# Kernel optimization log

Hardware: AMD Instinct MI355X
Metric: run time of the kernel (lower is better)

## Reference

```python
import jax, jax.numpy as jnp
import numpy as np
import math

MODEL_DIM = 1024
BATCH = 4
SEQ = 2048


def setup_inputs() -> dict:
    key = jax.random.key(0)
    kx, kq, kk, kv = jax.random.split(key, 4)
    x = jax.random.normal(kx, (BATCH, SEQ, MODEL_DIM), dtype=jnp.float32)
    # kaiming_uniform_(W.T, a=sqrt(5)) on a square matrix -> U(-b, b) with
    # b = sqrt(6 / ((1 + 5) * fan_in)) = 1/sqrt(model_dim)
    bound = 1.0 / math.sqrt(MODEL_DIM)
    Q = jax.random.uniform(kq, (MODEL_DIM, MODEL_DIM), jnp.float32, -bound, bound)
    K = jax.random.uniform(kk, (MODEL_DIM, MODEL_DIM), jnp.float32, -bound, bound)
    V = jax.random.uniform(kv, (MODEL_DIM, MODEL_DIM), jnp.float32, -bound, bound)
    # attention_input='both' => a = model_dim => F is the full identity mask
    F = jnp.eye(MODEL_DIM, dtype=jnp.float32)
    return {"x": x, "F": F, "Q": Q, "K": K, "V": V}


def reference(x, F, Q, K, V):
    # Qx = x @ F @ Q ; Kx = x @ F @ K ; Vx = x @ V
    xF = x @ F                      # [b, s, d]
    Qx = xF @ Q                     # [b, s, d]
    Kx = xF @ K                     # [b, s, d]
    Vx = x @ V                      # [b, s, d]
    scale = 1.0 / math.sqrt(MODEL_DIM)
    attn_scores = jnp.einsum('bsd,btd->bst', Qx, Kx) * scale  # [b, s, s]
    attn_probs = jax.nn.softmax(attn_scores, axis=-1)
    out = jnp.einsum('bst,btd->bsd', attn_probs, Vx)          # [b, s, d]
    return out
```

## Files before the change

### kernel.cpp

```cpp
#include <hip/hip_runtime.h>
#include <hip/hip_bf16.h>

using bf16 = __hip_bfloat16;
typedef __bf16 bf16x8 __attribute__((ext_vector_type(8)));
typedef float f32x4 __attribute__((ext_vector_type(4)));

#define AS3(p) ((__attribute__((address_space(3))) void*)(p))
#define AS1(p) ((const __attribute__((address_space(1))) void*)(p))

template <int W> __device__ __forceinline__ void waitv() {
  asm volatile("s_waitcnt vmcnt(%0)" ::"n"(W) : "memory");
}
#define BARR __builtin_amdgcn_s_barrier()
#define SCHEDB __builtin_amdgcn_sched_barrier(0)

__global__ void cast_f32_bf16_kernel(const float* __restrict__ in,
                                     bf16* __restrict__ out, int n4) {
  int i = blockIdx.x * blockDim.x + threadIdx.x;
  if (i >= n4) return;
  float4 v = reinterpret_cast<const float4*>(in)[i];
  union { ushort4 u; bf16 h[4]; } o;
  o.h[0] = __float2bfloat16(v.x);
  o.h[1] = __float2bfloat16(v.y);
  o.h[2] = __float2bfloat16(v.z);
  o.h[3] = __float2bfloat16(v.w);
  reinterpret_cast<ushort4*>(out)[i] = o.u;
}

__global__ void transpose3_kernel(const float* __restrict__ W0,
                                  const float* __restrict__ W1,
                                  const float* __restrict__ W2,
                                  bf16* __restrict__ out) {
  __shared__ bf16 tile[32][33];
  const float* in = (blockIdx.z == 0) ? W0 : (blockIdx.z == 1) ? W1 : W2;
  out += (long)blockIdx.z * 1024 * 1024;
  int c0 = blockIdx.x * 32, r0 = blockIdx.y * 32;
  for (int i = threadIdx.y; i < 32; i += 8)
    tile[i][threadIdx.x] = (bf16)in[(long)(r0 + i) * 1024 + c0 + threadIdx.x];
  __syncthreads();
  for (int i = threadIdx.y; i < 32; i += 8)
    out[(long)(c0 + i) * 1024 + r0 + threadIdx.x] = tile[threadIdx.x][i];
}

__device__ inline void store_c(float* p, float v) { *p = v; }
__device__ inline void store_c(bf16* p, float v) { *p = __float2bfloat16(v); }

template <int BN, int MODE, typename OutT>
__global__ __launch_bounds__(512, 1) void gemm2p_kernel(
    const bf16* __restrict__ A, const bf16* __restrict__ Bt, OutT* __restrict__ C,
    int K, int lda, int ldb, int ldc, long sAb, long sBb, long sCb,
    float* __restrict__ aux, int auxStride) {
  constexpr int BM = 256, BK = 64;
  constexpr int WN = (BN == 256) ? 4 : 2;
  constexpr int MF = (BN == 256) ? 8 : 4;
  constexpr int MCH = MF / 2;
  constexpr int NLA = 4;
  constexpr int NLB = BN / 64;
  constexpr int NL = NLA + NLB;
  constexpr int BUFELEM = (BM + BN) * BK;

  __shared__ alignas(16) bf16 lds[2 * BUFELEM];

  A += (long)blockIdx.z * sAb;
  Bt += (long)blockIdx.z * sBb;
  C += (long)blockIdx.z * sCb;
  if (MODE != 0) aux += (long)blockIdx.z * auxStride;
  const int tm = blockIdx.y * BM, tn = blockIdx.x * BN;
  const int tid = threadIdx.x, wv = tid >> 6, lane = tid & 63;
  const int wm = wv / WN, wn = wv % WN;
  const int r0 = wm * (MF * 16), c0 = wn * 64;
  const int lrow = lane & 15, lkc = lane >> 4;

  f32x4 acc[MF][4] = {};

  auto stage = [&](int buf, int kt) {
    bf16* base = lds + buf * BUFELEM;
#pragma unroll
    for (int i = 0; i < NLA; ++i) {
      int slot = i * 512 + tid;
      int row = slot >> 3;
      int cg = (slot & 7) ^ (row & 7);
      const bf16* src = A + (long)(tm + row) * lda + kt + cg * 8;
      __builtin_amdgcn_global_load_lds(AS1(src), AS3(base + slot * 8), 16, 0, 0);
    }
#pragma unroll
    for (int i = 0; i < NLB; ++i) {
      int slot = i * 512 + tid;
      int row = slot >> 3;
      int cg = (slot & 7) ^ (row & 7);
      const bf16* src = Bt + (long)(tn + row) * ldb + kt + cg * 8;
      __builtin_amdgcn_global_load_lds(AS1(src), AS3(base + BM * BK + slot * 8), 16, 0, 0);
    }
  };

  stage(0, 0);
  const int NT = K / BK;
  for (int t = 0; t < NT; ++t) {
    const int cur = t & 1;
    if (t + 1 < NT) {
      stage(cur ^ 1, (t + 1) * BK);
      waitv<NL>();
    } else {
      waitv<0>();
    }
    BARR;
    SCHEDB;

    const bf16* bA = lds + cur * BUFELEM;
    const bf16* bB = bA + BM * BK;

    bf16x8 bfr[4][2];
#pragma unroll
    for (int nj = 0; nj < 4; ++nj)
#pragma unroll
      for (int k = 0; k < 2; ++k) {
        int row = c0 + nj * 16 + lrow;
        int cx = (k * 4 + lkc) ^ (row & 7);
        bfr[nj][k] = *reinterpret_cast<const bf16x8*>(bB + row * 64 + cx * 8);
      }
#pragma unroll
    for (int ph = 0; ph < 2; ++ph) {
      bf16x8 afr[MCH][2];
#pragma unroll
      for (int mi = 0; mi < MCH; ++mi)
#pragma unroll
        for (int k = 0; k < 2; ++k) {
          int row = r0 + (ph * MCH + mi) * 16 + lrow;
          int cx = (k * 4 + lkc) ^ (row & 7);
          afr[mi][k] = *reinterpret_cast<const bf16x8*>(bA + row * 64 + cx * 8);
        }
      __builtin_amdgcn_s_setprio(1);
#pragma unroll
      for (int k = 0; k < 2; ++k)
#pragma unroll
        for (int mi = 0; mi < MCH; ++mi)
#pragma unroll
          for (int nj = 0; nj < 4; ++nj)
            acc[ph * MCH + mi][nj] = __builtin_amdgcn_mfma_f32_16x16x32_bf16(
                afr[mi][k], bfr[nj][k], acc[ph * MCH + mi][nj], 0, 0, 0);
      __builtin_amdgcn_s_setprio(0);
      SCHEDB;
      BARR;
      SCHEDB;
    }
  }

  const int crow = lkc * 4;
#pragma unroll
  for (int mi = 0; mi < MF; ++mi) {
#pragma unroll
    for (int r = 0; r < 4; ++r) {
      const int rowm = tm + r0 + mi * 16 + crow + r;
      OutT* cp = C + (long)rowm * ldc + tn + c0 + lrow;
      if (MODE == 0) {
#pragma unroll
        for (int nj = 0; nj < 4; ++nj) store_c(cp + nj * 16, acc[mi][nj][r]);
      } else if (MODE == 1) {
        float rs = 0.f;
#pragma unroll
        for (int nj = 0; nj < 4; ++nj) {
          float e = __expf(acc[mi][nj][r] * 0.03125f);
          rs += e;
          store_c(cp + nj * 16, e);
        }
        rs += __shfl_xor(rs, 1);
        rs += __shfl_xor(rs, 2);
        rs += __shfl_xor(rs, 4);
        rs += __shfl_xor(rs, 8);
        if ((lane & 15) == 0) atomicAdd(aux + rowm, rs);
      } else {
        float inv = 1.0f / aux[rowm];
#pragma unroll
        for (int nj = 0; nj < 4; ++nj) store_c(cp + nj * 16, acc[mi][nj][r] * inv);
      }
    }
  }
}

extern "C" void kernel_launch(void* const* d_in, const int* in_sizes, int n_in,
                              void* d_out, int out_size, void* d_ws, size_t ws_size,
                              hipStream_t stream) {
  const float* x = (const float*)d_in[0];
  const float* Wq = (const float*)d_in[2];
  const float* Wk = (const float*)d_in[3];
  const float* Wv = (const float*)d_in[4];
  float* out = (float*)d_out;

  const long D = 1024, S = 2048, B = 4, MS = B * S;

  bf16* xb  = (bf16*)d_ws;
  bf16* Wtc = xb + MS * D;
  bf16* QKx = Wtc + 3 * D * D;
  bf16* Vxt = QKx + MS * 2 * D;
  bf16* Sc  = Vxt + MS * D;
  float* rowsum = (float*)(Sc + B * S * S);

  dim3 blk(256);
  dim3 tblk(32, 8);

  cast_f32_bf16_kernel<<<(int)(MS * D / 4 / 256), blk, 0, stream>>>(x, xb, (int)(MS * D / 4));
  transpose3_kernel<<<dim3(32, 32, 3), tblk, 0, stream>>>(Wq, Wk, Wv, Wtc);
  gemm2p_kernel<128, 0, bf16><<<dim3(16, 32, 1), 512, 0, stream>>>(
      xb, Wtc, QKx, 1024, 1024, 1024, 2048, 0, 0, 0, nullptr, 0);
  gemm2p_kernel<128, 0, bf16><<<dim3(16, 4, 4), 512, 0, stream>>>(
      Wtc + 2 * D * D, xb, Vxt, 1024, 1024, 1024, 2048, 0, S * D, D * S, nullptr, 0);
  hipMemsetAsync(rowsum, 0, B * S * sizeof(float), stream);
  gemm2p_kernel<256, 1, bf16><<<dim3(8, 8, 4), 512, 0, stream>>>(
      QKx, QKx + D, Sc, 1024, 2048, 2048, 2048, S * 2 * D, S * 2 * D, S * S,
      rowsum, (int)S);
  gemm2p_kernel<128, 2, float><<<dim3(8, 8, 4), 512, 0, stream>>>(
      Sc, Vxt, out, 2048, 2048, 2048, 1024, S * S, D * S, S * D,
      rowsum, (int)S);
}
```

Before: 174.7 us.

## Add 256x256 GEMM kernel with 8-phase half-tile staging pipeline

Introduces a new GEMM kernel that splits each 256x256 tile's A and B k-slices into halves. Each half is staged separately, interleaving global-to-LDS loads with four MFMA phases and prefetching up to two k-steps ahead. It replaces the older kernel for the QK projection GEMM (now a 256-wide N tile) and for the score/exp GEMM. The aim is to hide load latency better and to increase reuse with larger tiles. The cost is more barriers per iteration and fewer blocks for the projection GEMM.

```diff
diff --git a/kernel.cpp b/kernel.cpp
--- a/kernel.cpp
+++ b/kernel.cpp
@@ -12,6 +12,7 @@
   asm volatile("s_waitcnt vmcnt(%0)" ::"n"(W) : "memory");
 }
 #define BARR __builtin_amdgcn_s_barrier()
+#define LGKM0 asm volatile("s_waitcnt lgkmcnt(0)" ::: "memory")
 #define SCHEDB __builtin_amdgcn_sched_barrier(0)
 
 __global__ void cast_f32_bf16_kernel(const float* __restrict__ in,
@@ -45,6 +46,160 @@
 __device__ inline void store_c(float* p, float v) { *p = v; }
 __device__ inline void store_c(bf16* p, float v) { *p = __float2bfloat16(v); }
 
+template <int MODE, typename OutT>
+__global__ __launch_bounds__(512, 1) void gemm8p_kernel(
+    const bf16* __restrict__ A, const bf16* __restrict__ Bt, OutT* __restrict__ C,
+    int K, int lda, int ldb, int ldc, long sAb, long sBb, long sCb,
+    float* __restrict__ aux, int auxStride) {
+  constexpr int HALF = 128 * 64;
+  constexpr int BB = 4 * HALF;
+  __shared__ alignas(16) bf16 lds[2 * BB];
+
+  A += (long)blockIdx.z * sAb;
+  Bt += (long)blockIdx.z * sBb;
+  C += (long)blockIdx.z * sCb;
+  if (MODE != 0) aux += (long)blockIdx.z * auxStride;
+  const int tm = blockIdx.y * 256, tn = blockIdx.x * 256;
+  const int tid = threadIdx.x, wv = tid >> 6, lane = tid & 63;
+  const int wm = wv >> 2, wn = wv & 3;
+  const int lrow = lane & 15, lkc = lane >> 4;
+
+  f32x4 acc[8][4] = {};
+  bf16x8 afr[4][2], bfr[2][2][2];
+
+  const int co0 = (lkc ^ (lrow & 7)) * 8;
+  const int co1 = ((4 + lkc) ^ (lrow & 7)) * 8;
+  const int arow = wm * 64 + lrow;
+  const int brow = wn * 32 + lrow;
+
+  auto stageA = [&](bf16* buf, int kt, int mh) {
+#pragma unroll
+    for (int i = 0; i < 2; ++i) {
+      int slot = i * 512 + tid;
+      int rp = slot >> 3;
+      int g = (rp & 63) | (mh << 6) | ((rp >> 6) << 7);
+      int cg = (slot & 7) ^ (rp & 7);
+      const bf16* src = A + (long)(tm + g) * lda + kt + cg * 8;
+      __builtin_amdgcn_global_load_lds(AS1(src), AS3(buf + mh * HALF + slot * 8), 16, 0, 0);
+    }
+  };
+  auto stageB = [&](bf16* buf, int kt, int nh) {
+#pragma unroll
+    for (int i = 0; i < 2; ++i) {
+      int slot = i * 512 + tid;
+      int rp = slot >> 3;
+      int g = (rp & 31) | (nh << 5) | ((rp >> 5) << 6);
+      int cg = (slot & 7) ^ (rp & 7);
+      const bf16* src = Bt + (long)(tn + g) * ldb + kt + cg * 8;
+      __builtin_amdgcn_global_load_lds(AS1(src),
+                                       AS3(buf + 2 * HALF + nh * HALF + slot * 8), 16, 0, 0);
+    }
+  };
+
+#define READ_A(MH)                                                          \
+  {                                                                         \
+    const bf16* pa = cur + (MH) * HALF;                                     \
+    _Pragma("unroll") for (int mi = 0; mi < 4; ++mi) {                      \
+      afr[mi][0] = *reinterpret_cast<const bf16x8*>(pa + (arow + mi * 16) * 64 + co0); \
+      afr[mi][1] = *reinterpret_cast<const bf16x8*>(pa + (arow + mi * 16) * 64 + co1); \
+    }                                                                       \
+  }
+#define READ_B(NH)                                                          \
+  {                                                                         \
+    const bf16* pb = cur + 2 * HALF + (NH) * HALF;                          \
+    _Pragma("unroll") for (int nj = 0; nj < 2; ++nj) {                      \
+      bfr[NH][nj][0] = *reinterpret_cast<const bf16x8*>(pb + (brow + nj * 16) * 64 + co0); \
+      bfr[NH][nj][1] = *reinterpret_cast<const bf16x8*>(pb + (brow + nj * 16) * 64 + co1); \
+    }                                                                       \
+  }
+#define MFMA_PH(MH, NH)                                                     \
+  __builtin_amdgcn_s_setprio(1);                                            \
+  _Pragma("unroll") for (int k = 0; k < 2; ++k)                             \
+      _Pragma("unroll") for (int mi = 0; mi < 4; ++mi)                      \
+          _Pragma("unroll") for (int nj = 0; nj < 2; ++nj)                  \
+    acc[(MH) * 4 + mi][(NH) * 2 + nj] =                                     \
+        __builtin_amdgcn_mfma_f32_16x16x32_bf16(                            \
+            afr[mi][k], bfr[NH][nj][k], acc[(MH) * 4 + mi][(NH) * 2 + nj],  \
+            0, 0, 0);                                                       \
+  __builtin_amdgcn_s_setprio(0);
+
+  const int NT = K / 64;
+  stageA(lds, 0, 0); stageB(lds, 0, 0);
+  stageA(lds, 0, 1); stageB(lds, 0, 1);
+  stageA(lds + BB, 64, 0); stageB(lds + BB, 64, 0);
+  waitv<8>();
+  BARR;
+
+  for (int t = 0; t < NT; ++t) {
+    const bf16* cur = lds + (t & 1) * BB;
+    bf16* nxt = lds + ((t & 1) ^ 1) * BB;
+    READ_A(0) READ_B(0)
+    SCHEDB;
+    if (t + 1 < NT) { stageA(nxt, (t + 1) * 64, 1); waitv<6>(); }
+    else waitv<0>();
+    BARR; LGKM0; SCHEDB;
+    MFMA_PH(0, 0)
+    SCHEDB; BARR;
+    READ_B(1)
+    SCHEDB;
+    if (t + 1 < NT) stageB(nxt, (t + 1) * 64, 1);
+    BARR; LGKM0; SCHEDB;
+    MFMA_PH(0, 1)
+    SCHEDB; BARR;
+    READ_A(1)
+    SCHEDB;
+    if (t + 2 < NT) stageA(nxt == lds ? (bf16*)lds + BB : (bf16*)lds, (t + 2) * 64, 0);
+    BARR; LGKM0; SCHEDB;
+    MFMA_PH(1, 0)
+    SCHEDB; BARR;
+    if (t + 2 < NT) {
+      stageB(nxt == lds ? (bf16*)lds + BB : (bf16*)lds, (t + 2) * 64, 0);
+      waitv<8>();
+    } else if (t + 1 < NT) {
+      waitv<4>();
+    }
+    BARR; SCHEDB;
+    MFMA_PH(1, 1)
+    SCHEDB; BARR;
+  }
+#undef READ_A
+#undef READ_B
+#undef MFMA_PH
+
+  const int crow = lkc * 4;
+#pragma unroll
+  for (int mh = 0; mh < 2; ++mh)
+#pragma unroll
+    for (int mi = 0; mi < 4; ++mi)
+#pragma unroll
+      for (int r = 0; r < 4; ++r) {
+        const int rowm = tm + wm * 128 + mh * 64 + mi * 16 + crow + r;
+        OutT* cp = C + (long)rowm * ldc + tn + wn * 64 + lrow;
+        if (MODE == 0) {
+#pragma unroll
+          for (int nh = 0; nh < 2; ++nh)
+#pragma unroll
+            for (int nj = 0; nj < 2; ++nj)
+              store_c(cp + nh * 32 + nj * 16, acc[mh * 4 + mi][nh * 2 + nj][r]);
+        } else {
+          float rs = 0.f;
+#pragma unroll
+          for (int nh = 0; nh < 2; ++nh)
+#pragma unroll
+            for (int nj = 0; nj < 2; ++nj) {
+              float e = __expf(acc[mh * 4 + mi][nh * 2 + nj][r] * 0.03125f);
+              rs += e;
+              store_c(cp + nh * 32 + nj * 16, e);
+            }
+          rs += __shfl_xor(rs, 1);
+          rs += __shfl_xor(rs, 2);
+          rs += __shfl_xor(rs, 4);
+          rs += __shfl_xor(rs, 8);
+          if ((lane & 15) == 0) atomicAdd(aux + rowm, rs);
+        }
+      }
+}
+
 template <int BN, int MODE, typename OutT>
 __global__ __launch_bounds__(512, 1) void gemm2p_kernel(
     const bf16* __restrict__ A, const bf16* __restrict__ Bt, OutT* __restrict__ C,
@@ -200,12 +355,12 @@
 
   cast_f32_bf16_kernel<<<(int)(MS * D / 4 / 256), blk, 0, stream>>>(x, xb, (int)(MS * D / 4));
   transpose3_kernel<<<dim3(32, 32, 3), tblk, 0, stream>>>(Wq, Wk, Wv, Wtc);
-  gemm2p_kernel<128, 0, bf16><<<dim3(16, 32, 1), 512, 0, stream>>>(
+  gemm8p_kernel<0, bf16><<<dim3(8, 32, 1), 512, 0, stream>>>(
       xb, Wtc, QKx, 1024, 1024, 1024, 2048, 0, 0, 0, nullptr, 0);
   gemm2p_kernel<128, 0, bf16><<<dim3(16, 4, 4), 512, 0, stream>>>(
       Wtc + 2 * D * D, xb, Vxt, 1024, 1024, 1024, 2048, 0, S * D, D * S, nullptr, 0);
   hipMemsetAsync(rowsum, 0, B * S * sizeof(float), stream);
-  gemm2p_kernel<256, 1, bf16><<<dim3(8, 8, 4), 512, 0, stream>>>(
+  gemm8p_kernel<1, bf16><<<dim3(8, 8, 4), 512, 0, stream>>>(
       QKx, QKx + D, Sc, 1024, 2048, 2048, 2048, S * 2 * D, S * 2 * D, S * S,
       rowsum, (int)S);
   gemm2p_kernel<128, 2, float><<<dim3(8, 8, 4), 512, 0, stream>>>(
```

Result: faster. 168.2 us (-3.7%).
